# Kernel optimization log

Measured on AMD Instinct MI355X. Metric: run time of the kernel, lower is better.

## Reference

```python
import jax, jax.numpy as jnp
import numpy as np

N_DIM = 32  # latent_dim + action_dim

# Static index sets matching the original Python loop order (i<=j, i<=j<=k)
_PI, _PJ = np.triu_indices(N_DIM)  # row-major i then j, matches loop order
_TRIPLES = np.array([(a, b, c) for a in range(N_DIM)
                     for b in range(a, N_DIM)
                     for c in range(b, N_DIM)], dtype=np.int32)
_TI, _TJ, _TK = _TRIPLES[:, 0], _TRIPLES[:, 1], _TRIPLES[:, 2]


def setup_inputs() -> dict:
    key = jax.random.key(0)
    z = jax.random.normal(key, (8192, N_DIM), dtype=jnp.float32)
    return {"z": z}


def reference(z):
    B = z.shape[0]
    ones = jnp.ones((B, 1), dtype=z.dtype)
    pairs = z[:, _PI] * z[:, _PJ]                      # (B, 528)
    triples = z[:, _TI] * z[:, _TJ] * z[:, _TK]        # (B, 5984)
    library = jnp.concatenate([ones, z, pairs, triples, jnp.sin(z)], axis=1)
    return library  # (B, 6577)
```

## Files before the change

kernel.cpp:

```cpp
#include <hip/hip_runtime.h>
#include <math.h>

#define NDIM   32
#define NPAIRS 528
#define NTRIP  5984
#define NCOLS  (1 + NDIM + NPAIRS + NTRIP + NDIM)
#define ULEN   593
#define ZOFF   528
#define SOFF   560
#define ONEOFF 592

struct Tbl  { unsigned v[NCOLS]; };
struct PTbl { unsigned v[NPAIRS]; };

constexpr unsigned pidx(int a, int b) {
    return (unsigned)(a * NDIM - a * (a - 1) / 2 + (b - a));
}

constexpr Tbl make_tbl() {
    Tbl t{}; int c = 0;
    t.v[c++] = ONEOFF | (ONEOFF << 10);
    for (int i = 0; i < NDIM; ++i)
        t.v[c++] = (ZOFF + i) | (ONEOFF << 10);
    for (int i = 0; i < NDIM; ++i)
        for (int j = i; j < NDIM; ++j)
            t.v[c++] = pidx(i, j) | (ONEOFF << 10);
    for (int a = 0; a < NDIM; ++a)
        for (int b = a; b < NDIM; ++b)
            for (int k = b; k < NDIM; ++k)
                t.v[c++] = pidx(a, b) | ((unsigned)(ZOFF + k) << 10);
    for (int i = 0; i < NDIM; ++i)
        t.v[c++] = (SOFF + i) | (ONEOFF << 10);
    return t;
}

constexpr PTbl make_ptbl() {
    PTbl t{}; int c = 0;
    for (int i = 0; i < NDIM; ++i)
        for (int j = i; j < NDIM; ++j)
            t.v[c++] = (unsigned)i | ((unsigned)j << 8);
    return t;
}

__device__ __constant__ Tbl  TBL  = make_tbl();
__device__ __constant__ PTbl PTBL = make_ptbl();

__global__ __launch_bounds__(256)
void sindy_kernel(const float* __restrict__ z, float* __restrict__ out) {
    __shared__ float u[4 * ULEN];
    const int tid  = threadIdx.x;
    const int row0 = blockIdx.x * 4;

    if (tid < 128) {
        const int r = tid >> 5, i = tid & 31;
        const float v = z[(row0 + r) * NDIM + i];
        u[r * ULEN + ZOFF + i] = v;
        u[r * ULEN + SOFF + i] = sinf(v);
        if (i == 0) u[r * ULEN + ONEOFF] = 1.0f;
    }
    __syncthreads();

#pragma unroll
    for (int r = 0; r < 4; ++r) {
        const float* ur = u + r * ULEN;
        for (int p = tid; p < NPAIRS; p += 256) {
            const unsigned e = PTBL.v[p];
            u[r * ULEN + p] = ur[ZOFF + (e & 255u)] * ur[ZOFF + (e >> 8)];
        }
    }
    __syncthreads();

    float* const outb = out + (long long)row0 * NCOLS;
    for (int t = tid; t < NCOLS; t += 256) {
        const int flat = t * 4;
        int r   = flat / NCOLS;
        int col = flat - r * NCOLS;
        const float* ur = u + r * ULEN;
        float v[4];
#pragma unroll
        for (int j = 0; j < 4; ++j) {
            const unsigned e = TBL.v[col];
            v[j] = ur[e & 1023u] * ur[(e >> 10) & 1023u];
            if (++col == NCOLS) { col = 0; ur += ULEN; }
        }
        *reinterpret_cast<float4*>(outb + flat) = make_float4(v[0], v[1], v[2], v[3]);
    }
}

extern "C" void kernel_launch(void* const* d_in, const int* in_sizes, int n_in,
                              void* d_out, int out_size, void* d_ws, size_t ws_size,
                              hipStream_t stream) {
    const float* z = (const float*)d_in[0];
    float* out     = (float*)d_out;
    const int rows   = in_sizes[0] / NDIM;
    const int blocks = rows / 4;
    sindy_kernel<<<blocks, 256, 0, stream>>>(z, out);
}
```

Baseline: 255.6 us.

## Cache column index table in registers and process eight rows per block

Each thread now loads its 26 column-table entries into registers once and reuses them across 8 rows per block, instead of re-reading the constant table per output element. Rows per block go from 4 to 8, the shared-memory row stride is padded to 608, and index fields widen to 12 bits. The output stores change from float4 vectors to per-thread scalar stores along each row. This adds register pressure and gives up the wide stores in exchange for fewer table lookups and no per-element division.

```diff
diff --git a/kernel.cpp b/kernel.cpp
--- a/kernel.cpp
+++ b/kernel.cpp
@@ -3,12 +3,13 @@
 
 #define NDIM   32
 #define NPAIRS 528
-#define NTRIP  5984
-#define NCOLS  (1 + NDIM + NPAIRS + NTRIP + NDIM)
-#define ULEN   593
+#define NCOLS  6577
+#define PAD    608
 #define ZOFF   528
 #define SOFF   560
 #define ONEOFF 592
+#define RPB    8
+#define NSLOT  26
 
 struct Tbl  { unsigned v[NCOLS]; };
 struct PTbl { unsigned v[NPAIRS]; };
@@ -19,18 +20,18 @@
 
 constexpr Tbl make_tbl() {
     Tbl t{}; int c = 0;
-    t.v[c++] = ONEOFF | (ONEOFF << 10);
+    t.v[c++] = ONEOFF | (ONEOFF << 12);
     for (int i = 0; i < NDIM; ++i)
-        t.v[c++] = (ZOFF + i) | (ONEOFF << 10);
+        t.v[c++] = (unsigned)(ZOFF + i) | (ONEOFF << 12);
     for (int i = 0; i < NDIM; ++i)
         for (int j = i; j < NDIM; ++j)
-            t.v[c++] = pidx(i, j) | (ONEOFF << 10);
+            t.v[c++] = pidx(i, j) | (ONEOFF << 12);
     for (int a = 0; a < NDIM; ++a)
         for (int b = a; b < NDIM; ++b)
             for (int k = b; k < NDIM; ++k)
-                t.v[c++] = pidx(a, b) | ((unsigned)(ZOFF + k) << 10);
+                t.v[c++] = pidx(a, b) | ((unsigned)(ZOFF + k) << 12);
     for (int i = 0; i < NDIM; ++i)
-        t.v[c++] = (SOFF + i) | (ONEOFF << 10);
+        t.v[c++] = (unsigned)(SOFF + i) | (ONEOFF << 12);
     return t;
 }
 
@@ -47,43 +48,46 @@
 
 __global__ __launch_bounds__(256)
 void sindy_kernel(const float* __restrict__ z, float* __restrict__ out) {
-    __shared__ float u[4 * ULEN];
+    __shared__ float u[RPB * PAD];
     const int tid  = threadIdx.x;
-    const int row0 = blockIdx.x * 4;
+    const int row0 = blockIdx.x * RPB;
 
-    if (tid < 128) {
-        const int r = tid >> 5, i = tid & 31;
-        const float v = z[(row0 + r) * NDIM + i];
-        u[r * ULEN + ZOFF + i] = v;
-        u[r * ULEN + SOFF + i] = sinf(v);
-        if (i == 0) u[r * ULEN + ONEOFF] = 1.0f;
+    unsigned idx[NSLOT];
+#pragma unroll
+    for (int j = 0; j < NSLOT; ++j) {
+        const int c = tid + 256 * j;
+        idx[j] = TBL.v[c < NCOLS ? c : 0];
+    }
+
+    {
+        const int r = tid >> 5, d = tid & 31;
+        const float v = z[(row0 + r) * NDIM + d];
+        u[r * PAD + ZOFF + d] = v;
+        u[r * PAD + SOFF + d] = sinf(v);
+        if (tid < RPB) u[tid * PAD + ONEOFF] = 1.0f;
     }
     __syncthreads();
 
-#pragma unroll
-    for (int r = 0; r < 4; ++r) {
-        const float* ur = u + r * ULEN;
-        for (int p = tid; p < NPAIRS; p += 256) {
-            const unsigned e = PTBL.v[p];
-            u[r * ULEN + p] = ur[ZOFF + (e & 255u)] * ur[ZOFF + (e >> 8)];
-        }
+    for (int p = tid; p < RPB * NPAIRS; p += 256) {
+        const int r = p / NPAIRS;
+        const int q = p - r * NPAIRS;
+        const unsigned e = PTBL.v[q];
+        const float* ur = u + r * PAD + ZOFF;
+        u[r * PAD + q] = ur[e & 255u] * ur[e >> 8];
     }
     __syncthreads();
 
-    float* const outb = out + (long long)row0 * NCOLS;
-    for (int t = tid; t < NCOLS; t += 256) {
-        const int flat = t * 4;
-        int r   = flat / NCOLS;
-        int col = flat - r * NCOLS;
-        const float* ur = u + r * ULEN;
-        float v[4];
+    for (int r = 0; r < RPB; ++r) {
+        const float* __restrict__ ur = u + r * PAD;
+        float* __restrict__ ro = out + (size_t)(row0 + r) * NCOLS;
 #pragma unroll
-        for (int j = 0; j < 4; ++j) {
-            const unsigned e = TBL.v[col];
-            v[j] = ur[e & 1023u] * ur[(e >> 10) & 1023u];
-            if (++col == NCOLS) { col = 0; ur += ULEN; }
+        for (int j = 0; j < NSLOT; ++j) {
+            const int c = tid + 256 * j;
+            if (j < NSLOT - 1 || c < NCOLS) {
+                const unsigned e = idx[j];
+                ro[c] = ur[e & 4095u] * ur[e >> 12];
+            }
         }
-        *reinterpret_cast<float4*>(outb + flat) = make_float4(v[0], v[1], v[2], v[3]);
     }
 }
 
@@ -93,6 +97,6 @@
     const float* z = (const float*)d_in[0];
     float* out     = (float*)d_out;
     const int rows   = in_sizes[0] / NDIM;
-    const int blocks = rows / 4;
+    const int blocks = rows / RPB;
     sindy_kernel<<<blocks, 256, 0, stream>>>(z, out);
 }
```

Measured after the change: 211.3 us. 17.3% less time.
